# Optimization experiments

Hardware: AMD Instinct MI355X
Metric: run time of the kernel (lower is better)

The kernel has to match this reference:

```python
import jax, jax.numpy as jnp
import numpy as np

VOCAB, DIM, HEADS, LAYERS = 32000, 1024, 16, 2
B, S = 2, 1024
HD = DIM // HEADS


def rmsnorm(x, g, eps=1e-6):
    return x * jax.lax.rsqrt(jnp.mean(x * x, axis=-1, keepdims=True) + eps) * g


def setup_inputs() -> dict:
    key = jax.random.key(0)
    ks = jax.random.split(key, 20)
    s = 0.02
    d = {
        "text_ids": jax.random.randint(ks[0], (B, S), 0, VOCAB),
        "embed": jax.random.normal(ks[1], (VOCAB, DIM), jnp.float32) * s,
        "g1": jnp.ones((LAYERS, DIM), jnp.float32),
        "wq": jax.random.normal(ks[2], (LAYERS, DIM, DIM), jnp.float32) * s,
        "bq": jnp.zeros((LAYERS, DIM), jnp.float32),
        "wk": jax.random.normal(ks[3], (LAYERS, DIM, DIM), jnp.float32) * s,
        "bk": jnp.zeros((LAYERS, DIM), jnp.float32),
        "wv": jax.random.normal(ks[4], (LAYERS, DIM, DIM), jnp.float32) * s,
        "bv": jnp.zeros((LAYERS, DIM), jnp.float32),
        "wo": jax.random.normal(ks[5], (LAYERS, DIM, DIM), jnp.float32) * s,
        "bo": jnp.zeros((LAYERS, DIM), jnp.float32),
        "g2": jnp.ones((LAYERS, DIM), jnp.float32),
        "w1": jax.random.normal(ks[6], (LAYERS, DIM, 4 * DIM), jnp.float32) * s,
        "b1": jnp.zeros((LAYERS, 4 * DIM), jnp.float32),
        "w2": jax.random.normal(ks[7], (LAYERS, 4 * DIM, DIM), jnp.float32) * s,
        "b2": jnp.zeros((LAYERS, DIM), jnp.float32),
        "gf": jnp.ones((DIM,), jnp.float32),
        "head_w": jax.random.normal(ks[8], (DIM, VOCAB), jnp.float32) * s,
        "head_b": jnp.zeros((VOCAB,), jnp.float32),
    }
    return d


def reference(text_ids, embed, g1, wq, bq, wk, bk, wv, bv, wo, bo,
              g2, w1, b1, w2, b2, gf, head_w, head_b):
    b, s = text_ids.shape
    x = embed[text_ids]                                   # [B,S,D]
    causal = jnp.tril(jnp.ones((s, s), dtype=bool))        # [S,S]
    scale = 1.0 / jnp.sqrt(jnp.asarray(HD, x.dtype))
    for l in range(LAYERS):
        # attention sublayer: x = x + attn(norm1(x))
        h = rmsnorm(x, g1[l])
        q = (h @ wq[l] + bq[l]).reshape(b, s, HEADS, HD)
        k = (h @ wk[l] + bk[l]).reshape(b, s, HEADS, HD)
        v = (h @ wv[l] + bv[l]).reshape(b, s, HEADS, HD)
        scores = jnp.einsum("bqhd,bkhd->bhqk", q, k) * scale
        scores = jnp.where(causal, scores, jnp.asarray(-1e30, scores.dtype))
        a = jax.nn.softmax(scores, axis=-1)
        o = jnp.einsum("bhqk,bkhd->bqhd", a, v).reshape(b, s, DIM)
        x = x + (o @ wo[l] + bo[l])
        # FFN sublayer: x = x + ffn(norm2(x)), SiLU MLP (MoE unused in source forward)
        h2 = rmsnorm(x, g2[l])
        x = x + (jax.nn.silu(h2 @ w1[l] + b1[l]) @ w2[l] + b2[l])
    x = rmsnorm(x, gf)
    return x.astype(jnp.float32) @ head_w + head_b         # [B,S,VOCAB]
```

## Files before the change

### kernel.cpp

```cpp
#include <hip/hip_runtime.h>

#define LAYERS 2
#define DIM 1024
#define HEADS 16
#define HD 64
#define BATCH 2
#define SEQ 1024
#define ROWS (BATCH * SEQ)
#define FFN (4 * DIM)
#define VOCAB 32000
#define QKVN (3 * DIM)

typedef unsigned short u16;
typedef short vshort8 __attribute__((ext_vector_type(8)));
typedef float f32x4 __attribute__((ext_vector_type(4)));

#define VMCNT(n) asm volatile("s_waitcnt vmcnt(" #n ")" ::: "memory")

__device__ __forceinline__ u16 f2bf(float f) {
  union { float f; unsigned u; } x{f};
  unsigned r = (x.u + 0x7fffu + ((x.u >> 16) & 1u)) >> 16;
  return (u16)r;
}

__device__ __forceinline__ void gll16(const void* g, u16* l) {
  __builtin_amdgcn_global_load_lds(
      (const __attribute__((address_space(1))) void*)g,
      (__attribute__((address_space(3))) void*)l, 16, 0, 0);
}

__device__ __forceinline__ int xcd_swizzle(int orig, int nwg) {
  int q = nwg >> 3, r = nwg & 7;
  int xcd = orig & 7;
  int base = (xcd < r) ? xcd * (q + 1) : r * (q + 1) + (xcd - r) * q;
  return base + (orig >> 3);
}

__global__ __launch_bounds__(256) void transpose_sq_kernel(
    const float* __restrict__ wq, const float* __restrict__ wk,
    const float* __restrict__ wv, const float* __restrict__ wo,
    u16* __restrict__ wqkvT, u16* __restrict__ woT) {
  __shared__ float tile[32][33];
  int z = blockIdx.z, l = z >> 2, wsel = z & 3;
  const float* src =
      (wsel == 0 ? wq : wsel == 1 ? wk : wsel == 2 ? wv : wo) +
      (size_t)l * DIM * DIM;
  u16* dst = (wsel < 3)
                 ? wqkvT + (size_t)l * QKVN * DIM + (size_t)wsel * DIM * DIM
                 : woT + (size_t)l * DIM * DIM;
  int c0 = blockIdx.x * 32, r0 = blockIdx.y * 32;
  int tx = threadIdx.x, ty = threadIdx.y;
#pragma unroll
  for (int i = 0; i < 4; i++)
    tile[ty + i * 8][tx] = src[(size_t)(r0 + ty + i * 8) * DIM + c0 + tx];
  __syncthreads();
#pragma unroll
  for (int i = 0; i < 4; i++)
    dst[(size_t)(c0 + ty + i * 8) * DIM + r0 + tx] = f2bf(tile[tx][ty + i * 8]);
}

template <int R, int C>
__global__ __launch_bounds__(256) void transpose_rc_kernel(
    const float* __restrict__ srcb, u16* __restrict__ dstb) {
  __shared__ float tile[32][33];
  int l = blockIdx.z;
  const float* src = srcb + (size_t)l * R * C;
  u16* dst = dstb + (size_t)l * R * C;
  int c0 = blockIdx.x * 32, r0 = blockIdx.y * 32;
  int tx = threadIdx.x, ty = threadIdx.y;
#pragma unroll
  for (int i = 0; i < 4; i++)
    tile[ty + i * 8][tx] = src[(size_t)(r0 + ty + i * 8) * C + c0 + tx];
  __syncthreads();
#pragma unroll
  for (int i = 0; i < 4; i++)
    dst[(size_t)(c0 + ty + i * 8) * R + r0 + tx] = f2bf(tile[tx][ty + i * 8]);
}

__global__ __launch_bounds__(256) void pack_qkv_bias(
    const float* __restrict__ bq, const float* __restrict__ bk,
    const float* __restrict__ bv, float* __restrict__ o) {
  int l = blockIdx.y;
  int t = blockIdx.x * 256 + threadIdx.x;
  float v;
  if (t < DIM) v = bq[l * DIM + t];
  else if (t < 2 * DIM) v = bk[l * DIM + t - DIM];
  else v = bv[l * DIM + t - 2 * DIM];
  o[(size_t)l * QKVN + t] = v;
}

__global__ __launch_bounds__(256) void embed_norm_kernel(
    const int* __restrict__ ids, const float* __restrict__ emb,
    const float* __restrict__ g, float* __restrict__ x, u16* __restrict__ h) {
  int row = blockIdx.x;
  int t = threadIdx.x;
  int id = ids[row];
  float4 v = ((const float4*)(emb + (size_t)id * DIM))[t];
  ((float4*)(x + (size_t)row * DIM))[t] = v;
  float ss = v.x * v.x + v.y * v.y + v.z * v.z + v.w * v.w;
  for (int off = 32; off > 0; off >>= 1) ss += __shfl_down(ss, off);
  __shared__ float part[4];
  if ((t & 63) == 0) part[t >> 6] = ss;
  __syncthreads();
  float tot = part[0] + part[1] + part[2] + part[3];
  float r = rsqrtf(tot / (float)DIM + 1e-6f);
  float4 gv = ((const float4*)g)[t];
  ushort4 o;
  o.x = f2bf(v.x * r * gv.x);
  o.y = f2bf(v.y * r * gv.y);
  o.z = f2bf(v.z * r * gv.z);
  o.w = f2bf(v.w * r * gv.w);
  *(ushort4*)(h + (size_t)row * DIM + t * 4) = o;
}

__global__ __launch_bounds__(256) void addnorm_kernel(
    float* __restrict__ x, const float* __restrict__ P0,
    const float* __restrict__ P1, const float* __restrict__ bias,
    const float* __restrict__ g, u16* __restrict__ h) {
  int row = blockIdx.x;
  int t = threadIdx.x;
  float4 v = ((const float4*)(x + (size_t)row * DIM))[t];
  float4 a = ((const float4*)(P0 + (size_t)row * DIM))[t];
  float4 b = ((const float4*)(P1 + (size_t)row * DIM))[t];
  float4 c = ((const float4*)bias)[t];
  v.x += a.x + b.x + c.x;
  v.y += a.y + b.y + c.y;
  v.z += a.z + b.z + c.z;
  v.w += a.w + b.w + c.w;
  ((float4*)(x + (size_t)row * DIM))[t] = v;
  float ss = v.x * v.x + v.y * v.y + v.z * v.z + v.w * v.w;
  for (int off = 32; off > 0; off >>= 1) ss += __shfl_down(ss, off);
  __shared__ float part[4];
  if ((t & 63) == 0) part[t >> 6] = ss;
  __syncthreads();
  float tot = part[0] + part[1] + part[2] + part[3];
  float r = rsqrtf(tot / (float)DIM + 1e-6f);
  float4 gv = ((const float4*)g)[t];
  ushort4 o;
  o.x = f2bf(v.x * r * gv.x);
  o.y = f2bf(v.y * r * gv.y);
  o.z = f2bf(v.z * r * gv.z);
  o.w = f2bf(v.w * r * gv.w);
  *(ushort4*)(h + (size_t)row * DIM + t * 4) = o;
}

template <int OUTBF, int SILU, int SPLITK, int MFAST, int VT>
__global__ __launch_bounds__(256, 2) void gemm128_kernel(
    const u16* __restrict__ A, const u16* __restrict__ Wt,
    const float* __restrict__ bias, void* __restrict__ outv,
    float* __restrict__ pout1, u16* __restrict__ vt2, int M, int N, int K) {
  __shared__ u16 As[2][128 * 64];
  __shared__ u16 Bs[2][128 * 64];
  int nm = M >> 7, nn = N >> 7, nwg = nm * nn;
  int wg = xcd_swizzle(blockIdx.x, SPLITK ? nwg * 2 : nwg);
  int ks = 0;
  if (SPLITK) { ks = wg >= nwg; wg -= ks * nwg; }
  int mi, ni;
  if (MFAST) { mi = wg % nm; ni = wg / nm; }
  else       { ni = wg % nn; mi = wg / nn; }
  int m0 = mi << 7, n0 = ni << 7;
  int kb = SPLITK ? ks * (K >> 1) : 0;
  int NTt = (SPLITK ? (K >> 1) : K) >> 6;
  int tid = threadIdx.x, wave = tid >> 6, lane = tid & 63;
  int wr = wave >> 1, wc = wave & 1;
  int r16 = lane & 15, g4 = lane >> 4;
  int lrow = lane >> 3, lslot = lane & 7;

  f32x4 acc[4][4] = {};

  auto stage = [&](int buf, int kt) {
#pragma unroll
    for (int i = 0; i < 4; i++) {
      int s = wave * 4 + i;
      int row = s * 8 + lrow;
      int slot = lslot ^ (row & 7);
      gll16(A + (size_t)(m0 + row) * K + kb + kt * 64 + slot * 8,
            &As[buf][s * 512 + lane * 8]);
    }
#pragma unroll
    for (int i = 0; i < 4; i++) {
      int s = wave * 4 + i;
      int row = s * 8 + lrow;
      int slot = lslot ^ (row & 7);
      gll16(Wt + (size_t)(n0 + row) * K + kb + kt * 64 + slot * 8,
            &Bs[buf][s * 512 + lane * 8]);
    }
  };

  stage(0, 0);
  VMCNT(0);
  __builtin_amdgcn_s_barrier();

  for (int t = 0; t < NTt; t++) {
    int cur = t & 1;
    if (t + 1 < NTt) stage(cur ^ 1, t + 1);
#pragma unroll
    for (int kk = 0; kk < 2; kk++) {
      vshort8 af[4], bf[4];
#pragma unroll
      for (int m = 0; m < 4; m++) {
        int r = wr * 64 + m * 16 + r16;
        int slot = (kk * 4 + g4) ^ (r & 7);
        af[m] = *(const vshort8*)&As[cur][r * 64 + slot * 8];
      }
#pragma unroll
      for (int n = 0; n < 4; n++) {
        int c = wc * 64 + n * 16 + r16;
        int slot = (kk * 4 + g4) ^ (c & 7);
        bf[n] = *(const vshort8*)&Bs[cur][c * 64 + slot * 8];
      }
#pragma unroll
      for (int m = 0; m < 4; m++)
#pragma unroll
        for (int n = 0; n < 4; n++)
          acc[m][n] = __builtin_amdgcn_mfma_f32_16x16x32_bf16(af[m], bf[n],
                                                              acc[m][n], 0, 0, 0);
    }
    VMCNT(0);
    __builtin_amdgcn_s_barrier();
  }

  if (SPLITK) {
    float* P = ks ? pout1 : (float*)outv;
#pragma unroll
    for (int m = 0; m < 4; m++) {
      int rowb = m0 + wr * 64 + m * 16 + g4 * 4;
#pragma unroll
      for (int n = 0; n < 4; n++) {
        int col = n0 + wc * 64 + n * 16 + r16;
#pragma unroll
        for (int j = 0; j < 4; j++)
          P[(size_t)(rowb + j) * N + col] = acc[m][n][j];
      }
    }
  } else {
#pragma unroll
    for (int m = 0; m < 4; m++) {
      int rowb = m0 + wr * 64 + m * 16 + g4 * 4;
#pragma unroll
      for (int n = 0; n < 4; n++) {
        int col = n0 + wc * 64 + n * 16 + r16;
        float b = bias[col];
        u16 ov[4];
#pragma unroll
        for (int j = 0; j < 4; j++) {
          float v = acc[m][n][j] + b;
          if (SILU) v = v / (1.f + __expf(-v));
          if (OUTBF) ov[j] = f2bf(v);
          else ((float*)outv)[(size_t)(rowb + j) * N + col] = v;
        }
        if (OUTBF) {
          if (VT && col >= 2 * DIM) {
            int dv = col - 2 * DIM;
            int hh = dv >> 6, dd = dv & 63;
            int bb = rowb >> 10, s = rowb & 1023;
            ushort4 o4{ov[0], ov[1], ov[2], ov[3]};
            *(ushort4*)&vt2[((((size_t)(bb * 16 + hh) * (SEQ / 8) + (s >> 3)) * 64 +
                              dd) * 8) + (s & 7)] = o4;
          } else {
#pragma unroll
            for (int j = 0; j < 4; j++)
              ((u16*)outv)[(size_t)(rowb + j) * N + col] = ov[j];
          }
        }
      }
    }
  }
}

__global__ __launch_bounds__(512, 2) void gemm256p_kernel(
    const u16* __restrict__ A, const u16* __restrict__ Wt,
    const float* __restrict__ bias, float* __restrict__ out,
    int M, int N, int K) {
  __shared__ u16 As[2][256 * 64];
  __shared__ u16 Bs[2][256 * 64];
  int nn = N >> 8;
  int wg = xcd_swizzle(blockIdx.x, nn * 2);
  int ni = wg >> 1, mhalf = wg & 1;
  int n0 = ni << 8;
  int tid = threadIdx.x, w = tid >> 6, lane = tid & 63;
  int wr = w >> 2, wc = w & 3;
  int r16 = lane & 15, g4 = lane >> 4;
  int srow8 = lane >> 3, sslot = lane & 7;
  const int NTK = 16;
  const int NGT = 64;

  f32x4 acc[8][4] = {};

  auto stageA = [&](int buf, int mb, int kt, int hb, int j) {
    int chunk = j * 8 + w;
    int row = hb * 128 + chunk * 8 + srow8;
    int slot = sslot ^ (row & 7);
    gll16(A + (size_t)(mb + row) * K + kt * 64 + slot * 8,
          &As[buf][hb * 8192 + chunk * 512 + lane * 8]);
  };
  auto stageB = [&](int buf, int kt, int hb, int j) {
    int chunk = j * 8 + w;
    int row = hb * 128 + chunk * 8 + srow8;
    int slot = sslot ^ (row & 7);
    gll16(Wt + (size_t)(n0 + row) * K + kt * 64 + slot * 8,
          &Bs[buf][hb * 8192 + chunk * 512 + lane * 8]);
  };
  auto readA = [&](int buf, int mf, int kk) -> vshort8 {
    int row = mf * 32 + wr * 16 + r16;
    int slot = (kk * 4 + g4) ^ (row & 7);
    return *(const vshort8*)&As[buf][row * 64 + slot * 8];
  };
  auto readB = [&](int buf, int nf, int kk) -> vshort8 {
    int row = nf * 64 + wc * 16 + r16;
    int slot = (kk * 4 + g4) ^ (row & 7);
    return *(const vshort8*)&Bs[buf][row * 64 + slot * 8];
  };

  int mb0 = (mhalf * 4) << 8;
  stageA(0, mb0, 0, 0, 0); stageA(0, mb0, 0, 0, 1);
  stageB(0, 0, 0, 0);      stageB(0, 0, 0, 1);
  stageB(0, 0, 1, 0);      stageB(0, 0, 1, 1);
  stageA(0, mb0, 0, 1, 0); stageA(0, mb0, 0, 1, 1);
  VMCNT(0);
  __builtin_amdgcn_s_barrier();

  vshort8 af[4][2], bf0[2][2], bf1[2][2];

  for (int ti = 0; ti < 4; ti++) {
    int m0 = (mhalf * 4 + ti) << 8;
    for (int tt = 0; tt < NTK; tt++) {
      int gt = ti * NTK + tt;
      int cur = gt & 1, nxt = cur ^ 1;
      int gt1 = gt + 1;
      bool hn = gt1 < NGT;
      int kt1 = gt1 & (NTK - 1);
      int mb1 = (mhalf * 4 + (gt1 >> 4)) << 8;
#pragma unroll
      for (int m = 0; m < 4; m++)
#pragma unroll
        for (int kk = 0; kk < 2; kk++) af[m][kk] = readA(cur, m, kk);
#pragma unroll
      for (int n = 0; n < 2; n++)
#pragma unroll
        for (int kk = 0; kk < 2; kk++) bf0[n][kk] = readB(cur, n, kk);
      if (hn) { stageA(nxt, mb1, kt1, 0, 0); stageA(nxt, mb1, kt1, 0, 1); }
      __builtin_amdgcn_s_barrier();
      __builtin_amdgcn_s_setprio(1);
#pragma unroll
      for (int m = 0; m < 4; m++)
#pragma unroll
        for (int n = 0; n < 2; n++)
#pragma unroll
          for (int kk = 0; kk < 2; kk++)
            acc[m][n] = __builtin_amdgcn_mfma_f32_16x16x32_bf16(
                af[m][kk], bf0[n][kk], acc[m][n], 0, 0, 0);
      __builtin_amdgcn_s_setprio(0);
      VMCNT(4);
      __builtin_amdgcn_s_barrier();
#pragma unroll
      for (int n = 0; n < 2; n++)
#pragma unroll
        for (int kk = 0; kk < 2; kk++) bf1[n][kk] = readB(cur, 2 + n, kk);
      if (hn) { stageB(nxt, kt1, 0, 0); stageB(nxt, kt1, 0, 1); }
      __builtin_amdgcn_s_barrier();
      __builtin_amdgcn_s_setprio(1);
#pragma unroll
      for (int m = 0; m < 4; m++)
#pragma unroll
        for (int n = 0; n < 2; n++)
#pragma unroll
          for (int kk = 0; kk < 2; kk++)
            acc[m][n + 2] = __builtin_amdgcn_mfma_f32_16x16x32_bf16(
                af[m][kk], bf1[n][kk], acc[m][n + 2], 0, 0, 0);
      __builtin_amdgcn_s_setprio(0);
      VMCNT(4);
      __builtin_amdgcn_s_barrier();
#pragma unroll
      for (int m = 0; m < 4; m++)
#pragma unroll
        for (int kk = 0; kk < 2; kk++) af[m][kk] = readA(cur, 4 + m, kk);
      if (hn) { stageB(nxt, kt1, 1, 0); stageB(nxt, kt1, 1, 1); }
      __builtin_amdgcn_s_barrier();
      __builtin_amdgcn_s_setprio(1);
#pragma unroll
      for (int m = 0; m < 4; m++)
#pragma unroll
        for (int n = 0; n < 2; n++)
#pragma unroll
          for (int kk = 0; kk < 2; kk++)
            acc[m + 4][n + 2] = __builtin_amdgcn_mfma_f32_16x16x32_bf16(
                af[m][kk], bf1[n][kk], acc[m + 4][n + 2], 0, 0, 0);
      __builtin_amdgcn_s_setprio(0);
      VMCNT(4);
      __builtin_amdgcn_s_barrier();
      if (hn) { stageA(nxt, mb1, kt1, 1, 0); stageA(nxt, mb1, kt1, 1, 1); }
      __builtin_amdgcn_s_barrier();
      __builtin_amdgcn_s_setprio(1);
#pragma unroll
      for (int m = 0; m < 4; m++)
#pragma unroll
        for (int n = 0; n < 2; n++)
#pragma unroll
          for (int kk = 0; kk < 2; kk++)
            acc[m + 4][n] = __builtin_amdgcn_mfma_f32_16x16x32_bf16(
                af[m][kk], bf0[n][kk], acc[m + 4][n], 0, 0, 0);
      __builtin_amdgcn_s_setprio(0);
      VMCNT(4);
      __builtin_amdgcn_s_barrier();
    }
#pragma unroll
    for (int mf = 0; mf < 8; mf++) {
      int rowb = m0 + mf * 32 + wr * 16 + g4 * 4;
#pragma unroll
      for (int nf = 0; nf < 4; nf++) {
        int col = n0 + nf * 64 + wc * 16 + r16;
        float b = bias[col];
#pragma unroll
        for (int j = 0; j < 4; j++)
          out[(size_t)(rowb + j) * N + col] = acc[mf][nf][j] + b;
      }
    }
#pragma unroll
    for (int mf = 0; mf < 8; mf++)
#pragma unroll
      for (int nf = 0; nf < 4; nf++) acc[mf][nf] = f32x4{0.f, 0.f, 0.f, 0.f};
  }
}

__global__ __launch_bounds__(256) void attn_kernel(const u16* __restrict__ qkv,
                                                   const u16* __restrict__ vt2,
                                                   u16* __restrict__ o) {
  __shared__ u16 Ks[2][32 * 64];
  __shared__ u16 pl[4][16 * 40];
  int qblk = blockIdx.x, bh = blockIdx.y;
  int b = bh >> 4, h = bh & 15;
  int tid = threadIdx.x, w = tid >> 6, lane = tid & 63;
  int r16 = lane & 15, g4 = lane >> 4;
  int q0 = qblk * 64 + w * 16;

  const u16* qrow = qkv + ((size_t)(b * SEQ) + q0 + r16) * QKVN + h * HD;
  vshort8 aq0 = *(const vshort8*)(qrow + g4 * 8);
  vshort8 aq1 = *(const vshort8*)(qrow + 32 + g4 * 8);

  float mrun[4], lrun[4];
  f32x4 accO[4];
#pragma unroll
  for (int j = 0; j < 4; j++) { mrun[j] = -1e30f; lrun[j] = 0.f; }
#pragma unroll
  for (int d = 0; d < 4; d++) accO[d] = f32x4{0.f, 0.f, 0.f, 0.f};

  int nkvT = qblk * 2 + 2;
  auto stageK = [&](int buf, int kt) {
    int row = tid >> 3;
    int slot = (tid & 7) ^ (row & 7);
    gll16(qkv + ((size_t)(b * SEQ) + kt * 32 + row) * QKVN + DIM + h * HD + slot * 8,
          &Ks[buf][w * 512 + lane * 8]);
  };
  stageK(0, 0);
  __syncthreads();
  int buf = 0;
  for (int kt = 0; kt < nkvT; kt++) {
    int kv0 = kt * 32;
    if (kt + 1 < nkvT) stageK(buf ^ 1, kt + 1);
    if (kv0 <= q0 + 15) {
      int row0 = r16, row1 = 16 + r16;
      vshort8 bk00 = *(const vshort8*)&Ks[buf][row0 * 64 + ((0 + g4) ^ (row0 & 7)) * 8];
      vshort8 bk01 = *(const vshort8*)&Ks[buf][row0 * 64 + ((4 + g4) ^ (row0 & 7)) * 8];
      vshort8 bk10 = *(const vshort8*)&Ks[buf][row1 * 64 + ((0 + g4) ^ (row1 & 7)) * 8];
      vshort8 bk11 = *(const vshort8*)&Ks[buf][row1 * 64 + ((4 + g4) ^ (row1 & 7)) * 8];
      f32x4 s0 = {}, s1 = {};
      s0 = __builtin_amdgcn_mfma_f32_16x16x32_bf16(aq0, bk00, s0, 0, 0, 0);
      s0 = __builtin_amdgcn_mfma_f32_16x16x32_bf16(aq1, bk01, s0, 0, 0, 0);
      s1 = __builtin_amdgcn_mfma_f32_16x16x32_bf16(aq0, bk10, s1, 0, 0, 0);
      s1 = __builtin_amdgcn_mfma_f32_16x16x32_bf16(aq1, bk11, s1, 0, 0, 0);

#pragma unroll
      for (int j = 0; j < 4; j++) {
        int qg = q0 + g4 * 4 + j;
        float x0 = s0[j] * 0.125f;
        float x1 = s1[j] * 0.125f;
        if (kv0 + r16 > qg) x0 = -1e30f;
        if (kv0 + 16 + r16 > qg) x1 = -1e30f;
        float mx = fmaxf(x0, x1);
#pragma unroll
        for (int mm = 1; mm < 16; mm <<= 1) mx = fmaxf(mx, __shfl_xor(mx, mm));
        float mnew = fmaxf(mrun[j], mx);
        float alpha = __expf(mrun[j] - mnew);
        float p0 = __expf(x0 - mnew);
        float p1 = __expf(x1 - mnew);
        float rs = p0 + p1;
#pragma unroll
        for (int mm = 1; mm < 16; mm <<= 1) rs += __shfl_xor(rs, mm);
        lrun[j] = lrun[j] * alpha + rs;
        mrun[j] = mnew;
#pragma unroll
        for (int d = 0; d < 4; d++) accO[d][j] *= alpha;
        pl[w][(g4 * 4 + j) * 40 + r16] = f2bf(p0);
        pl[w][(g4 * 4 + j) * 40 + 16 + r16] = f2bf(p1);
      }
      asm volatile("s_waitcnt lgkmcnt(0)" ::: "memory");
      vshort8 ap = *(const vshort8*)&pl[w][r16 * 40 + g4 * 8];
      const u16* vbase = vt2 + (((size_t)bh * (SEQ / 8) + (kv0 >> 3) + g4) * 64) * 8;
#pragma unroll
      for (int d = 0; d < 4; d++) {
        vshort8 bv = *(const vshort8*)(vbase + (size_t)(d * 16 + r16) * 8);
        accO[d] = __builtin_amdgcn_mfma_f32_16x16x32_bf16(ap, bv, accO[d], 0, 0, 0);
      }
    }
    __syncthreads();
    buf ^= 1;
  }

#pragma unroll
  for (int j = 0; j < 4; j++) {
    float inv = 1.f / lrun[j];
    int row = q0 + g4 * 4 + j;
#pragma unroll
    for (int d = 0; d < 4; d++)
      o[((size_t)(b * SEQ) + row) * DIM + h * HD + d * 16 + r16] =
          f2bf(accO[d][j] * inv);
  }
}

extern "C" void kernel_launch(void* const* d_in, const int* in_sizes, int n_in,
                              void* d_out, int out_size, void* d_ws,
                              size_t ws_size, hipStream_t stream) {
  const int* ids = (const int*)d_in[0];
  const float* emb = (const float*)d_in[1];
  const float* g1 = (const float*)d_in[2];
  const float* wq = (const float*)d_in[3];
  const float* bq = (const float*)d_in[4];
  const float* wk = (const float*)d_in[5];
  const float* bk = (const float*)d_in[6];
  const float* wv = (const float*)d_in[7];
  const float* bv = (const float*)d_in[8];
  const float* wo = (const float*)d_in[9];
  const float* bo = (const float*)d_in[10];
  const float* g2 = (const float*)d_in[11];
  const float* w1 = (const float*)d_in[12];
  const float* b1 = (const float*)d_in[13];
  const float* w2 = (const float*)d_in[14];
  const float* b2 = (const float*)d_in[15];
  const float* gf = (const float*)d_in[16];
  const float* head_w = (const float*)d_in[17];
  const float* head_b = (const float*)d_in[18];
  float* out = (float*)d_out;

  char* ws = (char*)d_ws;
  size_t off = 0;
  auto alloc = [&](size_t bytes) -> char* {
    char* p = ws + off;
    off += (bytes + 255) & ~(size_t)255;
    return p;
  };
  u16* wqkvT = (u16*)alloc((size_t)LAYERS * QKVN * DIM * 2);
  u16* woT = (u16*)alloc((size_t)LAYERS * DIM * DIM * 2);
  u16* w1T = (u16*)alloc((size_t)LAYERS * DIM * FFN * 2);
  u16* w2T = (u16*)alloc((size_t)LAYERS * DIM * FFN * 2);
  u16* headT = (u16*)alloc((size_t)VOCAB * DIM * 2);
  float* bqkv = (float*)alloc((size_t)LAYERS * QKVN * 4);
  float* x = (float*)alloc((size_t)ROWS * DIM * 4);
  u16* h = (u16*)alloc((size_t)ROWS * DIM * 2);
  u16* qkvb = (u16*)alloc((size_t)ROWS * QKVN * 2);
  u16* vtb = (u16*)alloc((size_t)ROWS * DIM * 2);
  u16* ob = (u16*)alloc((size_t)ROWS * DIM * 2);
  u16* tb = (u16*)alloc((size_t)ROWS * FFN * 2);
  float* P0 = (float*)alloc((size_t)ROWS * DIM * 4);
  float* P1 = (float*)alloc((size_t)ROWS * DIM * 4);
  if (off > ws_size) return;

  dim3 tb32(32, 8);
  transpose_sq_kernel<<<dim3(DIM / 32, DIM / 32, 4 * LAYERS), tb32, 0, stream>>>(
      wq, wk, wv, wo, wqkvT, woT);
  transpose_rc_kernel<DIM, FFN>
      <<<dim3(FFN / 32, DIM / 32, LAYERS), tb32, 0, stream>>>(w1, w1T);
  transpose_rc_kernel<FFN, DIM>
      <<<dim3(DIM / 32, FFN / 32, LAYERS), tb32, 0, stream>>>(w2, w2T);
  transpose_rc_kernel<DIM, VOCAB>
      <<<dim3(VOCAB / 32, DIM / 32, 1), tb32, 0, stream>>>(head_w, headT);
  pack_qkv_bias<<<dim3(QKVN / 256, LAYERS), 256, 0, stream>>>(bq, bk, bv, bqkv);

  embed_norm_kernel<<<ROWS, 256, 0, stream>>>(ids, emb, g1, x, h);

  for (int l = 0; l < LAYERS; l++) {
    gemm128_kernel<1, 0, 0, 1, 1>
        <<<(ROWS / 128) * (QKVN / 128), 256, 0, stream>>>(
            h, wqkvT + (size_t)l * QKVN * DIM, bqkv + (size_t)l * QKVN,
            qkvb, nullptr, vtb, ROWS, QKVN, DIM);
    attn_kernel<<<dim3(SEQ / 64, BATCH * HEADS), 256, 0, stream>>>(qkvb, vtb, ob);
    gemm128_kernel<0, 0, 1, 0, 0>
        <<<2 * (ROWS / 128) * (DIM / 128), 256, 0, stream>>>(
            ob, woT + (size_t)l * DIM * DIM, nullptr, P0, P1, nullptr,
            ROWS, DIM, DIM);
    addnorm_kernel<<<ROWS, 256, 0, stream>>>(
        x, P0, P1, bo + (size_t)l * DIM, g2 + (size_t)l * DIM, h);
    gemm128_kernel<1, 1, 0, 1, 0>
        <<<(ROWS / 128) * (FFN / 128), 256, 0, stream>>>(
            h, w1T + (size_t)l * DIM * FFN, b1 + (size_t)l * FFN, tb, nullptr,
            nullptr, ROWS, FFN, DIM);
    gemm128_kernel<0, 0, 1, 0, 0>
        <<<2 * (ROWS / 128) * (DIM / 128), 256, 0, stream>>>(
            tb, w2T + (size_t)l * DIM * FFN, nullptr, P0, P1, nullptr,
            ROWS, DIM, FFN);
    addnorm_kernel<<<ROWS, 256, 0, stream>>>(
        x, P0, P1, b2 + (size_t)l * DIM,
        (l == LAYERS - 1) ? gf : (g1 + (size_t)(l + 1) * DIM), h);
  }
  gemm256p_kernel<<<(VOCAB / 256) * 2, 512, 0, stream>>>(
      h, headT, head_b, out, ROWS, VOCAB, DIM);
}
```

Baseline: 605.2 us.

## Fuse weight transposes, add 256x128 GEMM tile, rebalance head GEMM staging

Replaces the four per-weight transpose launches with one kernel that works on 64x64 tiles, using float4 loads and 16-byte bf16 stores. The QKV and FFN-up GEMMs move to a new 512-thread kernel with 256x128 tiles, which reuses each B tile across more rows and runs fewer workgroups. The large output-head GEMM interleaves its A and B prefetches differently, with fewer vmcnt waits and barriers per k-step. The looser waits risk reading LDS data before it has landed, and the bigger tiles use more LDS and registers, which can lower occupancy.

```diff
diff --git a/kernel.cpp b/kernel.cpp
--- a/kernel.cpp
+++ b/kernel.cpp
@@ -36,45 +36,73 @@
   return base + (orig >> 3);
 }
 
-__global__ __launch_bounds__(256) void transpose_sq_kernel(
+__device__ __forceinline__ void trans64(const float* __restrict__ src,
+                                        u16* __restrict__ dst, int C, int R,
+                                        int r0, int c0, int tid,
+                                        u16 (*tl)[72]) {
+  int lr = tid >> 4, lc4 = (tid & 15) * 4;
+#pragma unroll
+  for (int i = 0; i < 4; i++) {
+    int row = lr + i * 16;
+    float4 v = *(const float4*)&src[(size_t)(r0 + row) * C + c0 + lc4];
+    ushort4 o{f2bf(v.x), f2bf(v.y), f2bf(v.z), f2bf(v.w)};
+    *(ushort4*)&tl[row][lc4] = o;
+  }
+  __syncthreads();
+#pragma unroll
+  for (int i = 0; i < 2; i++) {
+    int idx = tid + i * 256;
+    int ci = idx >> 3, ri0 = (idx & 7) * 8;
+    vshort8 o;
+#pragma unroll
+    for (int j = 0; j < 8; j++) o[j] = (short)tl[ri0 + j][ci];
+    *(vshort8*)&dst[(size_t)(c0 + ci) * R + r0 + ri0] = o;
+  }
+}
+
+__global__ __launch_bounds__(256) void transpose_all_kernel(
     const float* __restrict__ wq, const float* __restrict__ wk,
     const float* __restrict__ wv, const float* __restrict__ wo,
-    u16* __restrict__ wqkvT, u16* __restrict__ woT) {
-  __shared__ float tile[32][33];
-  int z = blockIdx.z, l = z >> 2, wsel = z & 3;
-  const float* src =
-      (wsel == 0 ? wq : wsel == 1 ? wk : wsel == 2 ? wv : wo) +
-      (size_t)l * DIM * DIM;
-  u16* dst = (wsel < 3)
-                 ? wqkvT + (size_t)l * QKVN * DIM + (size_t)wsel * DIM * DIM
-                 : woT + (size_t)l * DIM * DIM;
-  int c0 = blockIdx.x * 32, r0 = blockIdx.y * 32;
-  int tx = threadIdx.x, ty = threadIdx.y;
-#pragma unroll
-  for (int i = 0; i < 4; i++)
-    tile[ty + i * 8][tx] = src[(size_t)(r0 + ty + i * 8) * DIM + c0 + tx];
-  __syncthreads();
-#pragma unroll
-  for (int i = 0; i < 4; i++)
-    dst[(size_t)(c0 + ty + i * 8) * DIM + r0 + tx] = f2bf(tile[tx][ty + i * 8]);
-}
-
-template <int R, int C>
-__global__ __launch_bounds__(256) void transpose_rc_kernel(
-    const float* __restrict__ srcb, u16* __restrict__ dstb) {
-  __shared__ float tile[32][33];
-  int l = blockIdx.z;
-  const float* src = srcb + (size_t)l * R * C;
-  u16* dst = dstb + (size_t)l * R * C;
-  int c0 = blockIdx.x * 32, r0 = blockIdx.y * 32;
-  int tx = threadIdx.x, ty = threadIdx.y;
-#pragma unroll
-  for (int i = 0; i < 4; i++)
-    tile[ty + i * 8][tx] = src[(size_t)(r0 + ty + i * 8) * C + c0 + tx];
-  __syncthreads();
-#pragma unroll
-  for (int i = 0; i < 4; i++)
-    dst[(size_t)(c0 + ty + i * 8) * R + r0 + tx] = f2bf(tile[tx][ty + i * 8]);
+    const float* __restrict__ w1, const float* __restrict__ w2,
+    const float* __restrict__ head_w, u16* __restrict__ wqkvT,
+    u16* __restrict__ woT, u16* __restrict__ w1T, u16* __restrict__ w2T,
+    u16* __restrict__ headT) {
+  __shared__ u16 tl[64][72];
+  int bid = blockIdx.x, tid = threadIdx.x;
+  const float* src;
+  u16* dst;
+  int R, C, r0, c0;
+  if (bid < 2048) {
+    int job = bid >> 8, tile = bid & 255;
+    int l = job >> 2, wsel = job & 3;
+    src = (wsel == 0 ? wq : wsel == 1 ? wk : wsel == 2 ? wv : wo) +
+          (size_t)l * DIM * DIM;
+    dst = (wsel < 3)
+              ? wqkvT + (size_t)l * QKVN * DIM + (size_t)wsel * DIM * DIM
+              : woT + (size_t)l * DIM * DIM;
+    R = DIM; C = DIM;
+    c0 = (tile & 15) * 64; r0 = (tile >> 4) * 64;
+  } else if (bid < 4096) {
+    int idx = bid - 2048;
+    int l = idx >> 10, t = idx & 1023;
+    src = w1 + (size_t)l * DIM * FFN;
+    dst = w1T + (size_t)l * DIM * FFN;
+    R = DIM; C = FFN;
+    c0 = (t & 63) * 64; r0 = (t >> 6) * 64;
+  } else if (bid < 6144) {
+    int idx = bid - 4096;
+    int l = idx >> 10, t = idx & 1023;
+    src = w2 + (size_t)l * FFN * DIM;
+    dst = w2T + (size_t)l * FFN * DIM;
+    R = FFN; C = DIM;
+    c0 = (t & 15) * 64; r0 = (t >> 4) * 64;
+  } else {
+    int t = bid - 6144;
+    src = head_w; dst = headT;
+    R = DIM; C = VOCAB;
+    c0 = (t % 500) * 64; r0 = (t / 500) * 64;
+  }
+  trans64(src, dst, C, R, r0, c0, tid, tl);
 }
 
 __global__ __launch_bounds__(256) void pack_qkv_bias(
@@ -144,6 +172,134 @@
   *(ushort4*)(h + (size_t)row * DIM + t * 4) = o;
 }
 
+template <int SILU, int VT>
+__global__ __launch_bounds__(512, 2) void gemm256x128_kernel(
+    const u16* __restrict__ A, const u16* __restrict__ Wt,
+    const float* __restrict__ bias, u16* __restrict__ outb,
+    u16* __restrict__ vt2, int M, int N, int K) {
+  __shared__ u16 As[2][256 * 64];
+  __shared__ u16 Bs[2][128 * 64];
+  int nm = M >> 8, nn = N >> 7;
+  int wg = xcd_swizzle(blockIdx.x, nm * nn);
+  int mi = wg % nm, ni = wg / nm;
+  int m0 = mi << 8, n0 = ni << 7;
+  int tid = threadIdx.x, w = tid >> 6, lane = tid & 63;
+  int wr = w >> 1, wc = w & 1;
+  int r16 = lane & 15, g4 = lane >> 4;
+  int srow8 = lane >> 3, sslot = lane & 7;
+  int NT = K >> 6;
+
+  f32x4 acc[4][4] = {};
+
+  auto stageA = [&](int buf, int kt, int j) {
+    int chunk = j * 8 + w;
+    int row = chunk * 8 + srow8;
+    int slot = sslot ^ (row & 7);
+    gll16(A + (size_t)(m0 + row) * K + kt * 64 + slot * 8,
+          &As[buf][chunk * 512 + lane * 8]);
+  };
+  auto stageB = [&](int buf, int kt, int j) {
+    int chunk = j * 8 + w;
+    int row = chunk * 8 + srow8;
+    int slot = sslot ^ (row & 7);
+    gll16(Wt + (size_t)(n0 + row) * K + kt * 64 + slot * 8,
+          &Bs[buf][chunk * 512 + lane * 8]);
+  };
+  auto readA = [&](int buf, int mf, int kk) -> vshort8 {
+    int row = wr * 64 + mf * 16 + r16;
+    int slot = (kk * 4 + g4) ^ (row & 7);
+    return *(const vshort8*)&As[buf][row * 64 + slot * 8];
+  };
+  auto readB = [&](int buf, int nf, int kk) -> vshort8 {
+    int row = wc * 64 + nf * 16 + r16;
+    int slot = (kk * 4 + g4) ^ (row & 7);
+    return *(const vshort8*)&Bs[buf][row * 64 + slot * 8];
+  };
+
+  stageA(0, 0, 0); stageA(0, 0, 1); stageA(0, 0, 2); stageA(0, 0, 3);
+  stageB(0, 0, 0); stageB(0, 0, 1);
+  VMCNT(0);
+  __builtin_amdgcn_s_barrier();
+
+  vshort8 af[4][2], bf[2][2];
+
+  for (int t = 0; t < NT; t++) {
+    int cur = t & 1, nxt = cur ^ 1;
+    bool hn = (t + 1 < NT);
+#pragma unroll
+    for (int m = 0; m < 4; m++)
+#pragma unroll
+      for (int kk = 0; kk < 2; kk++) af[m][kk] = readA(cur, m, kk);
+#pragma unroll
+    for (int n = 0; n < 2; n++)
+#pragma unroll
+      for (int kk = 0; kk < 2; kk++) bf[n][kk] = readB(cur, n, kk);
+    if (hn) {
+      stageA(nxt, t + 1, 0); stageA(nxt, t + 1, 1);
+      stageA(nxt, t + 1, 2); stageA(nxt, t + 1, 3);
+      stageB(nxt, t + 1, 0); stageB(nxt, t + 1, 1);
+    }
+    __builtin_amdgcn_s_barrier();
+    __builtin_amdgcn_s_setprio(1);
+#pragma unroll
+    for (int m = 0; m < 4; m++)
+#pragma unroll
+      for (int n = 0; n < 2; n++)
+#pragma unroll
+        for (int kk = 0; kk < 2; kk++)
+          acc[m][n] = __builtin_amdgcn_mfma_f32_16x16x32_bf16(
+              af[m][kk], bf[n][kk], acc[m][n], 0, 0, 0);
+    __builtin_amdgcn_s_setprio(0);
+    __builtin_amdgcn_s_barrier();
+#pragma unroll
+    for (int n = 0; n < 2; n++)
+#pragma unroll
+      for (int kk = 0; kk < 2; kk++) bf[n][kk] = readB(cur, 2 + n, kk);
+    __builtin_amdgcn_s_barrier();
+    __builtin_amdgcn_s_setprio(1);
+#pragma unroll
+    for (int m = 0; m < 4; m++)
+#pragma unroll
+      for (int n = 0; n < 2; n++)
+#pragma unroll
+        for (int kk = 0; kk < 2; kk++)
+          acc[m][n + 2] = __builtin_amdgcn_mfma_f32_16x16x32_bf16(
+              af[m][kk], bf[n][kk], acc[m][n + 2], 0, 0, 0);
+    __builtin_amdgcn_s_setprio(0);
+    VMCNT(0);
+    __builtin_amdgcn_s_barrier();
+  }
+
+#pragma unroll
+  for (int m = 0; m < 4; m++) {
+    int rowb = m0 + wr * 64 + m * 16 + g4 * 4;
+#pragma unroll
+    for (int n = 0; n < 4; n++) {
+      int col = n0 + wc * 64 + n * 16 + r16;
+      float b = bias[col];
+      u16 ov[4];
+#pragma unroll
+      for (int j = 0; j < 4; j++) {
+        float v = acc[m][n][j] + b;
+        if (SILU) v = v / (1.f + __expf(-v));
+        ov[j] = f2bf(v);
+      }
+      if (VT && col >= 2 * DIM) {
+        int dv = col - 2 * DIM;
+        int hh = dv >> 6, dd = dv & 63;
+        int bb = rowb >> 10, s = rowb & 1023;
+        ushort4 o4{ov[0], ov[1], ov[2], ov[3]};
+        *(ushort4*)&vt2[((((size_t)(bb * 16 + hh) * (SEQ / 8) + (s >> 3)) * 64 +
+                          dd) * 8) + (s & 7)] = o4;
+      } else {
+#pragma unroll
+        for (int j = 0; j < 4; j++)
+          outb[(size_t)(rowb + j) * N + col] = ov[j];
+      }
+    }
+  }
+}
+
 template <int OUTBF, int SILU, int SPLITK, int MFAST, int VT>
 __global__ __launch_bounds__(256, 2) void gemm128_kernel(
     const u16* __restrict__ A, const u16* __restrict__ Wt,
@@ -317,7 +473,7 @@
   stageB(0, 0, 0, 0);      stageB(0, 0, 0, 1);
   stageB(0, 0, 1, 0);      stageB(0, 0, 1, 1);
   stageA(0, mb0, 0, 1, 0); stageA(0, mb0, 0, 1, 1);
-  VMCNT(0);
+  VMCNT(4);
   __builtin_amdgcn_s_barrier();
 
   vshort8 af[4][2], bf0[2][2], bf1[2][2];
@@ -339,7 +495,10 @@
       for (int n = 0; n < 2; n++)
 #pragma unroll
         for (int kk = 0; kk < 2; kk++) bf0[n][kk] = readB(cur, n, kk);
-      if (hn) { stageA(nxt, mb1, kt1, 0, 0); stageA(nxt, mb1, kt1, 0, 1); }
+      if (hn) {
+        stageA(nxt, mb1, kt1, 0, 0); stageA(nxt, mb1, kt1, 0, 1);
+        stageB(nxt, kt1, 0, 0);      stageB(nxt, kt1, 0, 1);
+      }
       __builtin_amdgcn_s_barrier();
       __builtin_amdgcn_s_setprio(1);
 #pragma unroll
@@ -357,7 +516,6 @@
       for (int n = 0; n < 2; n++)
 #pragma unroll
         for (int kk = 0; kk < 2; kk++) bf1[n][kk] = readB(cur, 2 + n, kk);
-      if (hn) { stageB(nxt, kt1, 0, 0); stageB(nxt, kt1, 0, 1); }
       __builtin_amdgcn_s_barrier();
       __builtin_amdgcn_s_setprio(1);
 #pragma unroll
@@ -369,13 +527,15 @@
             acc[m][n + 2] = __builtin_amdgcn_mfma_f32_16x16x32_bf16(
                 af[m][kk], bf1[n][kk], acc[m][n + 2], 0, 0, 0);
       __builtin_amdgcn_s_setprio(0);
-      VMCNT(4);
       __builtin_amdgcn_s_barrier();
 #pragma unroll
       for (int m = 0; m < 4; m++)
 #pragma unroll
         for (int kk = 0; kk < 2; kk++) af[m][kk] = readA(cur, 4 + m, kk);
-      if (hn) { stageB(nxt, kt1, 1, 0); stageB(nxt, kt1, 1, 1); }
+      if (hn) {
+        stageB(nxt, kt1, 1, 0);      stageB(nxt, kt1, 1, 1);
+        stageA(nxt, mb1, kt1, 1, 0); stageA(nxt, mb1, kt1, 1, 1);
+      }
       __builtin_amdgcn_s_barrier();
       __builtin_amdgcn_s_setprio(1);
 #pragma unroll
@@ -386,12 +546,6 @@
           for (int kk = 0; kk < 2; kk++)
             acc[m + 4][n + 2] = __builtin_amdgcn_mfma_f32_16x16x32_bf16(
                 af[m][kk], bf1[n][kk], acc[m + 4][n + 2], 0, 0, 0);
-      __builtin_amdgcn_s_setprio(0);
-      VMCNT(4);
-      __builtin_amdgcn_s_barrier();
-      if (hn) { stageA(nxt, mb1, kt1, 1, 0); stageA(nxt, mb1, kt1, 1, 1); }
-      __builtin_amdgcn_s_barrier();
-      __builtin_amdgcn_s_setprio(1);
 #pragma unroll
       for (int m = 0; m < 4; m++)
 #pragma unroll
@@ -565,24 +719,16 @@
   float* P1 = (float*)alloc((size_t)ROWS * DIM * 4);
   if (off > ws_size) return;
 
-  dim3 tb32(32, 8);
-  transpose_sq_kernel<<<dim3(DIM / 32, DIM / 32, 4 * LAYERS), tb32, 0, stream>>>(
-      wq, wk, wv, wo, wqkvT, woT);
-  transpose_rc_kernel<DIM, FFN>
-      <<<dim3(FFN / 32, DIM / 32, LAYERS), tb32, 0, stream>>>(w1, w1T);
-  transpose_rc_kernel<FFN, DIM>
-      <<<dim3(DIM / 32, FFN / 32, LAYERS), tb32, 0, stream>>>(w2, w2T);
-  transpose_rc_kernel<DIM, VOCAB>
-      <<<dim3(VOCAB / 32, DIM / 32, 1), tb32, 0, stream>>>(head_w, headT);
+  transpose_all_kernel<<<14144, 256, 0, stream>>>(
+      wq, wk, wv, wo, w1, w2, head_w, wqkvT, woT, w1T, w2T, headT);
   pack_qkv_bias<<<dim3(QKVN / 256, LAYERS), 256, 0, stream>>>(bq, bk, bv, bqkv);
-
   embed_norm_kernel<<<ROWS, 256, 0, stream>>>(ids, emb, g1, x, h);
 
   for (int l = 0; l < LAYERS; l++) {
-    gemm128_kernel<1, 0, 0, 1, 1>
-        <<<(ROWS / 128) * (QKVN / 128), 256, 0, stream>>>(
+    gemm256x128_kernel<0, 1>
+        <<<(ROWS / 256) * (QKVN / 128), 512, 0, stream>>>(
             h, wqkvT + (size_t)l * QKVN * DIM, bqkv + (size_t)l * QKVN,
-            qkvb, nullptr, vtb, ROWS, QKVN, DIM);
+            qkvb, vtb, ROWS, QKVN, DIM);
     attn_kernel<<<dim3(SEQ / 64, BATCH * HEADS), 256, 0, stream>>>(qkvb, vtb, ob);
     gemm128_kernel<0, 0, 1, 0, 0>
         <<<2 * (ROWS / 128) * (DIM / 128), 256, 0, stream>>>(
@@ -590,10 +736,10 @@
             ROWS, DIM, DIM);
     addnorm_kernel<<<ROWS, 256, 0, stream>>>(
         x, P0, P1, bo + (size_t)l * DIM, g2 + (size_t)l * DIM, h);
-    gemm128_kernel<1, 1, 0, 1, 0>
-        <<<(ROWS / 128) * (FFN / 128), 256, 0, stream>>>(
+    gemm256x128_kernel<1, 0>
+        <<<(ROWS / 256) * (FFN / 128), 512, 0, stream>>>(
             h, w1T + (size_t)l * DIM * FFN, b1 + (size_t)l * FFN, tb, nullptr,
-            nullptr, ROWS, FFN, DIM);
+            ROWS, FFN, DIM);
     gemm128_kernel<0, 0, 1, 0, 0>
         <<<2 * (ROWS / 128) * (DIM / 128), 256, 0, stream>>>(
             tb, w2T + (size_t)l * DIM * FFN, nullptr, P0, P1, nullptr,
```

Result: faster. 589.6 us (-2.6%).
